# Performance work log

Hardware: AMD Instinct MI355X
Metric: run time of the kernel (lower is better)

The kernel has to match this reference:

```python
import jax, jax.numpy as jnp
import numpy as np

MODEL_DIM = 2048
Q_HEADS = 32
KV_HEADS = 8
HEAD_DIM = MODEL_DIM // Q_HEADS  # 64
ROPE_BASE = 10000.0


def apply_rope(x, pos):
    # x: [B, S, H, D], interleaved-pair RoPE (torchtune-style)
    half = x.shape[-1] // 2
    inv_freq = 1.0 / (ROPE_BASE ** (jnp.arange(half, dtype=jnp.float32) * 2.0 / x.shape[-1]))
    ang = pos.astype(jnp.float32)[:, None] * inv_freq[None, :]        # [S, half]
    cos = jnp.cos(ang)[None, :, None, :]                              # [1,S,1,half]
    sin = jnp.sin(ang)[None, :, None, :]
    x1 = x[..., 0::2]
    x2 = x[..., 1::2]
    o1 = x1 * cos - x2 * sin
    o2 = x2 * cos + x1 * sin
    return jnp.stack([o1, o2], axis=-1).reshape(x.shape)


def setup_inputs() -> dict:
    key = jax.random.key(0)
    ks = jax.random.split(key, 5)
    B, S, D = 2, 2048, MODEL_DIM
    sd = 1.0 / np.sqrt(D)
    x = jax.random.normal(ks[0], (B, S, D), dtype=jnp.float32)
    wq = jax.random.normal(ks[1], (Q_HEADS * HEAD_DIM, D), dtype=jnp.float32) * sd
    wk = jax.random.normal(ks[2], (KV_HEADS * HEAD_DIM, D), dtype=jnp.float32) * sd
    wv = jax.random.normal(ks[3], (KV_HEADS * HEAD_DIM, D), dtype=jnp.float32) * sd
    wo = jax.random.normal(ks[4], (D, D), dtype=jnp.float32) * sd
    attention_mask = jnp.ones((B, S), dtype=bool)
    return {"x": x, "attention_mask": attention_mask, "wq": wq, "wk": wk, "wv": wv, "wo": wo}


def reference(x, attention_mask, wq, wk, wv, wo):
    B, S, D = x.shape
    rep = Q_HEADS // KV_HEADS
    q = (x @ wq.T).reshape(B, S, Q_HEADS, HEAD_DIM)
    k = (x @ wk.T).reshape(B, S, KV_HEADS, HEAD_DIM)
    v = (x @ wv.T).reshape(B, S, KV_HEADS, HEAD_DIM)
    # GQA repeat_interleave along head axis
    k = jnp.repeat(k, rep, axis=2)
    v = jnp.repeat(v, rep, axis=2)
    pos = jnp.arange(S)
    q = apply_rope(q, pos)
    k = apply_rope(k, pos)
    # scores [B, H, Sq, Sk]
    score = jnp.einsum('bqhd,bkhd->bhqk', q, k) / np.sqrt(HEAD_DIM)
    neg_inf = jnp.finfo(score.dtype).min
    causal = jnp.tril(jnp.ones((S, S), dtype=bool))
    score = jnp.where(causal[None, None, :, :], score, neg_inf)
    score = jnp.where(attention_mask[:, None, None, :], score, neg_inf)
    attn = jax.nn.softmax(score, axis=-1)
    out = jnp.einsum('bhqk,bkhd->bqhd', attn, v).reshape(B, S, D)
    return out @ wo.T
```

## Files before the change

### kernel.cpp

```cpp
#include <hip/hip_runtime.h>
#include <hip/hip_bf16.h>

#define S_LEN 2048
#define BATCH 2
#define DMODEL 2048
#define HQ 32
#define HKV 8
#define HD 64
#define NQ 2560
#define KDIM 2048

typedef __attribute__((ext_vector_type(8))) short bf16x8;
typedef __attribute__((ext_vector_type(4))) float f32x4;

#if __has_builtin(__builtin_amdgcn_exp2f)
#define EXP2(x) __builtin_amdgcn_exp2f(x)
#else
#define EXP2(x) exp2f(x)
#endif

template<int N> struct ic { static constexpr int value = N; };

static __device__ inline ushort f2bf(float f) {
    union { float f; unsigned u; } v; v.f = f;
    unsigned r = v.u + 0x7fff + ((v.u >> 16) & 1);
    return (ushort)(r >> 16);
}
static __device__ inline float bf2f(ushort h) {
    union { unsigned u; float f; } v; v.u = ((unsigned)h) << 16; return v.f;
}
static __device__ inline unsigned pack2(float lo, float hi) {
    return (unsigned)f2bf(lo) | ((unsigned)f2bf(hi) << 16);
}
static __device__ __forceinline__ unsigned pkbf(float lo, float hi) {
    union { float f; unsigned u; } a, b; a.f = lo; b.f = hi;
    return __builtin_amdgcn_perm(b.u + 0x8000u, a.u + 0x8000u, 0x07060302u);
}
static __device__ __forceinline__ unsigned cvtpk(float lo, float hi) {
    unsigned r;
    asm("v_cvt_pk_bf16_f32 %0, %1, %2" : "=v"(r) : "v"(lo), "v"(hi));
    return r;
}

static __device__ __forceinline__ void gload16(const ushort* g, ushort* l) {
    __builtin_amdgcn_global_load_lds(
        (const __attribute__((address_space(1))) unsigned int*)(g),
        (__attribute__((address_space(3))) unsigned int*)(l), 16, 0, 0);
}

#define BARRIER() asm volatile("s_barrier" ::: "memory")
#define WAITVM(N) asm volatile("s_waitcnt vmcnt(" #N ")" ::: "memory")

__global__ __launch_bounds__(256) void convert_kernel(const float* __restrict__ x,
                                                      const float* __restrict__ wq,
                                                      const float* __restrict__ wk,
                                                      const float* __restrict__ wv,
                                                      const float* __restrict__ wo,
                                                      ushort* __restrict__ xb,
                                                      ushort* __restrict__ wqkvb,
                                                      ushort* __restrict__ wob)
{
    size_t e = ((size_t)blockIdx.x * 256 + threadIdx.x) * 8;
    const float* src; ushort* dst;
    if (e < 8388608ul)       { src = x  + e;              dst = xb + e; }
    else if (e < 12582912ul) { src = wq + (e - 8388608);  dst = wqkvb + (e - 8388608); }
    else if (e < 13631488ul) { src = wk + (e - 12582912); dst = wqkvb + 4194304 + (e - 12582912); }
    else if (e < 14680064ul) { src = wv + (e - 13631488); dst = wqkvb + 5242880 + (e - 13631488); }
    else                     { src = wo + (e - 14680064); dst = wob + (e - 14680064); }
    float4 a = *(const float4*)src;
    float4 b = *(const float4*)(src + 4);
    uint4 p; p.x = pack2(a.x, a.y); p.y = pack2(a.z, a.w);
             p.z = pack2(b.x, b.y); p.w = pack2(b.z, b.w);
    *(uint4*)dst = p;
}

template<int BNF, int EPI>
__global__ __launch_bounds__(512, 2) void gemm256(const ushort* __restrict__ A,
                                                  const ushort* __restrict__ Bw,
                                                  ushort* __restrict__ qkv,
                                                  ushort* __restrict__ vT,
                                                  float* __restrict__ Cf)
{
    constexpr int BN = BNF * 64;
    constexpr int KT = KDIM / 64;
    __shared__ ushort As[2][256 * 64];
    __shared__ ushort Bs[2][BN * 64];
    const int t    = threadIdx.x;
    const int w    = t >> 6, lane = t & 63;
    const int quad = lane >> 4, l15 = lane & 15;
    const int l8   = lane >> 3;
    const int scw  = ((lane & 7) ^ (l8 & 7)) * 8;
    const int wm   = (w >> 2) * 128;
    const int wn   = (w & 3) * (BNF * 16);

    const int bid = blockIdx.x;
    const int sb  = (bid & 7) * 32 + (bid >> 3);
    const int mb  = (sb >> 4) * 256;
    const int nb  = (sb & 15) * BN;

    f32x4 acc[8][BNF] = {};
    bf16x8 a[4][2], b[BNF][2];

    auto SAH = [&](int buf, int half, int kb) {
        #pragma unroll
        for (int L = 0; L < 2; L++) {
            int r0 = half * 128 + (w * 2 + L) * 8;
            gload16(A + (size_t)(mb + r0 + l8) * KDIM + kb + scw, &As[buf][r0 * 64]);
        }
    };
    auto SB = [&](int buf, int kb) {
        #pragma unroll
        for (int L = 0; L < BNF; L++) {
            int r0 = (w * BNF + L) * 8;
            gload16(Bw + (size_t)(nb + r0 + l8) * KDIM + kb + scw, &Bs[buf][r0 * 64]);
        }
    };
    auto LA = [&](int buf, int hm) {
        #pragma unroll
        for (int i = 0; i < 4; i++) {
            int r = wm + hm * 64 + i * 16 + l15;
            int rs = r * 64, sw = r & 7;
            #pragma unroll
            for (int kc = 0; kc < 2; kc++)
                a[i][kc] = *(const bf16x8*)&As[buf][rs + (((kc << 2) | quad) ^ sw) * 8];
        }
    };
    auto LB = [&](int buf) {
        #pragma unroll
        for (int j = 0; j < BNF; j++) {
            int r = wn + j * 16 + l15;
            int rs = r * 64, sw = r & 7;
            #pragma unroll
            for (int kc = 0; kc < 2; kc++)
                b[j][kc] = *(const bf16x8*)&Bs[buf][rs + (((kc << 2) | quad) ^ sw) * 8];
        }
    };
    auto MM = [&](auto HM) {
        constexpr int hm = decltype(HM)::value;
        __builtin_amdgcn_s_setprio(1);
        #pragma unroll
        for (int i = 0; i < 4; i++)
            #pragma unroll
            for (int j = 0; j < BNF; j++) {
                f32x4 d = acc[hm * 4 + i][j];
                d = __builtin_amdgcn_mfma_f32_16x16x32_bf16(a[i][0], b[j][0], d, 0, 0, 0);
                d = __builtin_amdgcn_mfma_f32_16x16x32_bf16(a[i][1], b[j][1], d, 0, 0, 0);
                acc[hm * 4 + i][j] = d;
            }
        __builtin_amdgcn_s_setprio(0);
    };

    SAH(0, 0, 0); SAH(0, 1, 0); SB(0, 0);
    SAH(1, 0, 64); SB(1, 64);
    if constexpr (BNF == 3) WAITVM(5); else WAITVM(4);
    BARRIER();

    #pragma unroll 1
    for (int tt = 0; tt < KT - 2; tt++) {
        const int buf = tt & 1, o = buf ^ 1;
        LA(buf, 0); LB(buf);
        SAH(o, 1, (tt + 1) * 64);
        BARRIER();
        MM(ic<0>{});
        if constexpr (BNF == 3) WAITVM(7); else WAITVM(6);
        BARRIER();
        LA(buf, 1);
        SAH(buf, 0, (tt + 2) * 64); SB(buf, (tt + 2) * 64);
        BARRIER();
        MM(ic<1>{});
        if constexpr (BNF == 3) WAITVM(7); else WAITVM(6);
        BARRIER();
    }
    LA(0, 0); LB(0);
    SAH(1, 1, (KT - 1) * 64);
    BARRIER();
    MM(ic<0>{});
    if constexpr (BNF == 3) WAITVM(7); else WAITVM(6);
    BARRIER();
    LA(0, 1);
    BARRIER();
    MM(ic<1>{});
    WAITVM(2);
    BARRIER();
    LA(1, 0); LB(1);
    BARRIER();
    MM(ic<0>{});
    WAITVM(0);
    BARRIER();
    LA(1, 1);
    BARRIER();
    MM(ic<1>{});

    #pragma unroll
    for (int i = 0; i < 8; i++) {
        int m0 = mb + wm + (i >> 2) * 64 + (i & 3) * 16 + quad * 4;
        #pragma unroll
        for (int j = 0; j < BNF; j++) {
            int n0 = nb + wn + j * 16;
            if (EPI == 0) {
                if (n0 >= 2560) {
                    int m0p = (m0 & ~63) | (((m0 >> 5) & 1) << 5)
                            | (((m0 >> 2) & 3) << 3) | (((m0 >> 4) & 1) << 2);
                    ushort4 pk;
                    pk.x = f2bf(acc[i][j][0]); pk.y = f2bf(acc[i][j][1]);
                    pk.z = f2bf(acc[i][j][2]); pk.w = f2bf(acc[i][j][3]);
                    *(ushort4*)&vT[(size_t)(n0 + l15 - 2560) * 4096 + m0p] = pk;
                } else {
                    #pragma unroll
                    for (int r = 0; r < 4; r++)
                        qkv[(size_t)(m0 + r) * NQ + n0 + l15] = f2bf(acc[i][j][r]);
                }
            } else {
                #pragma unroll
                for (int r = 0; r < 4; r++)
                    Cf[(size_t)(m0 + r) * DMODEL + n0 + l15] = acc[i][j][r];
            }
        }
    }
}

__global__ __launch_bounds__(256) void rope_kernel(ushort* __restrict__ qkv)
{
    const int PAIRS = BATCH * S_LEN * (HQ + HKV) * (HD / 2);
    int tid = blockIdx.x * 256 + threadIdx.x;
    if (tid >= PAIRS) return;
    int token = tid / ((HQ + HKV) * 32);
    int r     = tid - token * ((HQ + HKV) * 32);
    int hh    = r >> 5;
    int i     = r & 31;
    int base  = (hh < HQ) ? hh * 64 : DMODEL + (hh - HQ) * 64;
    size_t addr = (size_t)token * NQ + base + 2 * i;
    int s = token & (S_LEN - 1);
    float freq = exp2f(-0.41524101186092f * (float)i);
    float ang  = (float)s * freq;
    float sn, cs;
    sincosf(ang, &sn, &cs);
    float x1 = bf2f(qkv[addr]);
    float x2 = bf2f(qkv[addr + 1]);
    qkv[addr]     = f2bf(x1 * cs - x2 * sn);
    qkv[addr + 1] = f2bf(x2 * cs + x1 * sn);
}

__global__ __launch_bounds__(256) void attn_kernel(const ushort* __restrict__ qkv,
                                                   const ushort* __restrict__ vT,
                                                   ushort* __restrict__ attnb)
{
    __shared__ ushort Ks[2][64 * 64];
    __shared__ ushort VT[2][64 * 64];
    const int t    = threadIdx.x;
    const int w    = t >> 6, lane = t & 63;
    const int quad = lane >> 4, l15 = lane & 15;
    const int bid  = blockIdx.x;
    const int qx   = 15 - (bid >> 6);
    const int h    = bid & 31;
    const int b    = (bid >> 5) & 1;
    const int qb   = qx * 128;
    const int kvh  = h >> 2;
    const ushort* base = qkv + (size_t)b * S_LEN * NQ;
    const ushort* vTb  = vT + (size_t)kvh * HD * 4096 + b * S_LEN;

    const float SC = 0.18033688011112042f;
    bf16x8 aq[2][2];
    #pragma unroll
    for (int h2 = 0; h2 < 2; h2++) {
        const ushort* qp = base + (size_t)(qb + w * 32 + h2 * 16 + l15) * NQ + h * HD + quad * 8;
        #pragma unroll
        for (int hf = 0; hf < 2; hf++) {
            bf16x8 v = *(const bf16x8*)(qp + hf * 32);
            #pragma unroll
            for (int j = 0; j < 8; j++) v[j] = (short)f2bf(bf2f((ushort)v[j]) * SC);
            aq[h2][hf] = v;
        }
    }

    f32x4 o[2][4] = {};
    float lsum[2] = {};
    const int qw    = qb + w * 32;
    const int strow = lane >> 3;
    const int stlc  = (lane & 7) ^ strow;
    const int niter = (qb + 128) / 64;

    #pragma unroll
    for (int c = 0; c < 2; c++) {
        int key = w * 16 + c * 8 + strow;
        gload16(base + (size_t)key * NQ + DMODEL + kvh * HD + stlc * 8,
                &Ks[0][(w * 16 + c * 8) * 64]);
        gload16(vTb + (size_t)key * 4096 + stlc * 8,
                &VT[0][(w * 16 + c * 8) * 64]);
    }

    for (int i = 0; i < niter; i++) {
        const int kb  = i * 64;
        const int cur = i & 1;
        __syncthreads();
        if (i + 1 < niter) {
            int kb2 = kb + 64;
            #pragma unroll
            for (int c = 0; c < 2; c++) {
                int key = w * 16 + c * 8 + strow;
                gload16(base + (size_t)(kb2 + key) * NQ + DMODEL + kvh * HD + stlc * 8,
                        &Ks[1 - cur][(w * 16 + c * 8) * 64]);
                gload16(vTb + (size_t)key * 4096 + kb2 + stlc * 8,
                        &VT[1 - cur][(w * 16 + c * 8) * 64]);
            }
        }
        if (kb <= qw + 31) {
            const bool full = (kb + 63) <= qw;
            const ushort* ks = &Ks[cur][0];
            const ushort* vs = &VT[cur][0];
            f32x4 s[2][4];
            #pragma unroll
            for (int kt = 0; kt < 4; kt++) {
                int key = kt * 16 + l15;
                int sw  = l15 & 7;
                bf16x8 k0 = *(const bf16x8*)&ks[key * 64 + (quad ^ sw) * 8];
                bf16x8 k1 = *(const bf16x8*)&ks[key * 64 + (((quad + 4) & 7) ^ sw) * 8];
                #pragma unroll
                for (int h2 = 0; h2 < 2; h2++) {
                    f32x4 z = {};
                    z = __builtin_amdgcn_mfma_f32_16x16x32_bf16(k0, aq[h2][0], z, 0, 0, 0);
                    z = __builtin_amdgcn_mfma_f32_16x16x32_bf16(k1, aq[h2][1], z, 0, 0, 0);
                    s[h2][kt] = z;
                }
            }
            bf16x8 pf[2][2];
            #pragma unroll
            for (int h2 = 0; h2 < 2; h2++) {
                union { unsigned u[8]; bf16x8 v[2]; } pw;
                #pragma unroll
                for (int kt = 0; kt < 4; kt++) {
                    float p0 = EXP2(s[h2][kt][0]);
                    float p1 = EXP2(s[h2][kt][1]);
                    float p2 = EXP2(s[h2][kt][2]);
                    float p3 = EXP2(s[h2][kt][3]);
                    if (!full) {
                        int key0 = kb + kt * 16 + quad * 4;
                        int q    = qb + w * 32 + h2 * 16 + l15;
                        p0 = (key0 + 0 <= q) ? p0 : 0.f;
                        p1 = (key0 + 1 <= q) ? p1 : 0.f;
                        p2 = (key0 + 2 <= q) ? p2 : 0.f;
                        p3 = (key0 + 3 <= q) ? p3 : 0.f;
                    }
                    lsum[h2] += (p0 + p1) + (p2 + p3);
                    pw.u[kt * 2 + 0] = cvtpk(p0, p1);
                    pw.u[kt * 2 + 1] = cvtpk(p2, p3);
                }
                pf[h2][0] = pw.v[0];
                pf[h2][1] = pw.v[1];
            }
            #pragma unroll
            for (int tt = 0; tt < 4; tt++) {
                int dr = tt * 16 + l15;
                int sw = l15 & 7;
                bf16x8 vf0 = *(const bf16x8*)&vs[dr * 64 + (quad ^ sw) * 8];
                bf16x8 vf1 = *(const bf16x8*)&vs[dr * 64 + (((quad + 4) & 7) ^ sw) * 8];
                #pragma unroll
                for (int h2 = 0; h2 < 2; h2++) {
                    f32x4 oo = o[h2][tt];
                    oo = __builtin_amdgcn_mfma_f32_16x16x32_bf16(vf0, pf[h2][0], oo, 0, 0, 0);
                    oo = __builtin_amdgcn_mfma_f32_16x16x32_bf16(vf1, pf[h2][1], oo, 0, 0, 0);
                    o[h2][tt] = oo;
                }
            }
        }
    }
    #pragma unroll
    for (int h2 = 0; h2 < 2; h2++) {
        float l = lsum[h2];
        l += __shfl_xor(l, 16, 64);
        l += __shfl_xor(l, 32, 64);
        float inv = 1.0f / l;
        ushort* ob = attnb + (size_t)(b * S_LEN + qb + w * 32 + h2 * 16 + l15) * DMODEL
                   + h * HD + quad * 4;
        #pragma unroll
        for (int tt = 0; tt < 4; tt++) {
            uint2 st;
            st.x = pkbf(o[h2][tt][0] * inv, o[h2][tt][1] * inv);
            st.y = pkbf(o[h2][tt][2] * inv, o[h2][tt][3] * inv);
            *(uint2*)&ob[tt * 16] = st;
        }
    }
}

extern "C" void kernel_launch(void* const* d_in, const int* in_sizes, int n_in,
                              void* d_out, int out_size, void* d_ws, size_t ws_size,
                              hipStream_t stream)
{
    const float* x  = (const float*)d_in[0];
    const float* wq = (const float*)d_in[2];
    const float* wk = (const float*)d_in[3];
    const float* wv = (const float*)d_in[4];
    const float* wo = (const float*)d_in[5];
    float* out = (float*)d_out;

    char* ws = (char*)d_ws;
    ushort* qkv    = (ushort*)(ws);
    ushort* vT     = (ushort*)(ws + 20971520);
    ushort* xb     = (ushort*)(ws + 25165824);
    ushort* attn_b = xb;
    ushort* wqkvb  = (ushort*)(ws + 41943040);
    ushort* wob    = (ushort*)(ws + 54525952);

    convert_kernel<<<9216, 256, 0, stream>>>(x, wq, wk, wv, wo, xb, wqkvb, wob);

    gemm256<3, 0><<<256, 512, 0, stream>>>(xb, wqkvb, qkv, vT, nullptr);

    int pairs = BATCH * S_LEN * (HQ + HKV) * (HD / 2);
    rope_kernel<<<(pairs + 255) / 256, 256, 0, stream>>>(qkv);

    attn_kernel<<<1024, 256, 0, stream>>>(qkv, vT, attn_b);

    gemm256<2, 1><<<256, 512, 0, stream>>>(attn_b, wob, nullptr, nullptr, out);
}
```

Baseline: 268.4 us.

## Triple-buffer K tiles and use explicit vmcnt waits in attention loop

```diff
diff --git a/kernel.cpp b/kernel.cpp
--- a/kernel.cpp
+++ b/kernel.cpp
@@ -245,7 +245,7 @@
                                                    const ushort* __restrict__ vT,
                                                    ushort* __restrict__ attnb)
 {
-    __shared__ ushort Ks[2][64 * 64];
+    __shared__ ushort Ks[3][64 * 64];
     __shared__ ushort VT[2][64 * 64];
     const int t    = threadIdx.x;
     const int w    = t >> 6, lane = t & 63;
@@ -280,34 +280,36 @@
     const int stlc  = (lane & 7) ^ strow;
     const int niter = (qb + 128) / 64;
 
-    #pragma unroll
-    for (int c = 0; c < 2; c++) {
-        int key = w * 16 + c * 8 + strow;
-        gload16(base + (size_t)key * NQ + DMODEL + kvh * HD + stlc * 8,
-                &Ks[0][(w * 16 + c * 8) * 64]);
-        gload16(vTb + (size_t)key * 4096 + stlc * 8,
-                &VT[0][(w * 16 + c * 8) * 64]);
-    }
-
+    auto stageK = [&](int i, int buf) {
+        #pragma unroll
+        for (int c = 0; c < 2; c++) {
+            int key = w * 16 + c * 8 + strow;
+            gload16(base + (size_t)(i * 64 + key) * NQ + DMODEL + kvh * HD + stlc * 8,
+                    &Ks[buf][(w * 16 + c * 8) * 64]);
+        }
+    };
+    auto stageV = [&](int i, int buf) {
+        #pragma unroll
+        for (int c = 0; c < 2; c++) {
+            int key = w * 16 + c * 8 + strow;
+            gload16(vTb + (size_t)key * 4096 + i * 64 + stlc * 8,
+                    &VT[buf][(w * 16 + c * 8) * 64]);
+        }
+    };
+
+    stageK(0, 0); stageV(0, 0); stageK(1, 1);
+
+    int kcur = 0, vcur = 0;
     for (int i = 0; i < niter; i++) {
-        const int kb  = i * 64;
-        const int cur = i & 1;
-        __syncthreads();
-        if (i + 1 < niter) {
-            int kb2 = kb + 64;
-            #pragma unroll
-            for (int c = 0; c < 2; c++) {
-                int key = w * 16 + c * 8 + strow;
-                gload16(base + (size_t)(kb2 + key) * NQ + DMODEL + kvh * HD + stlc * 8,
-                        &Ks[1 - cur][(w * 16 + c * 8) * 64]);
-                gload16(vTb + (size_t)key * 4096 + kb2 + stlc * 8,
-                        &VT[1 - cur][(w * 16 + c * 8) * 64]);
-            }
-        }
+        const int kb = i * 64;
+        if (i + 1 < niter) { WAITVM(2); } else { WAITVM(0); }
+        BARRIER();
+        if (i + 1 < niter) stageV(i + 1, vcur ^ 1);
+        if (i + 2 < niter) stageK(i + 2, kcur >= 1 ? kcur - 1 : 2);
         if (kb <= qw + 31) {
             const bool full = (kb + 63) <= qw;
-            const ushort* ks = &Ks[cur][0];
-            const ushort* vs = &VT[cur][0];
+            const ushort* ks = &Ks[kcur][0];
+            const ushort* vs = &VT[vcur][0];
             f32x4 s[2][4];
             #pragma unroll
             for (int kt = 0; kt < 4; kt++) {
@@ -363,6 +365,8 @@
                 }
             }
         }
+        kcur = (kcur + 1 == 3) ? 0 : kcur + 1;
+        vcur ^= 1;
     }
     #pragma unroll
     for (int h2 = 0; h2 < 2; h2++) {
```

Result: no change. 272.8 us (+1.6%).

## Use 256-row query blocks with 8 waves in attention kernel

Applied to the files above, without the earlier changes.

```diff
diff --git a/kernel.cpp b/kernel.cpp
--- a/kernel.cpp
+++ b/kernel.cpp
@@ -241,9 +241,9 @@
     qkv[addr + 1] = f2bf(x2 * cs + x1 * sn);
 }
 
-__global__ __launch_bounds__(256) void attn_kernel(const ushort* __restrict__ qkv,
-                                                   const ushort* __restrict__ vT,
-                                                   ushort* __restrict__ attnb)
+__global__ __launch_bounds__(512, 4) void attn_kernel(const ushort* __restrict__ qkv,
+                                                      const ushort* __restrict__ vT,
+                                                      ushort* __restrict__ attnb)
 {
     __shared__ ushort Ks[2][64 * 64];
     __shared__ ushort VT[2][64 * 64];
@@ -251,10 +251,11 @@
     const int w    = t >> 6, lane = t & 63;
     const int quad = lane >> 4, l15 = lane & 15;
     const int bid  = blockIdx.x;
-    const int qx   = 15 - (bid >> 6);
+    const int g    = bid >> 6;
+    const int qs   = (g < 4) ? 7 - g : g - 4;
     const int h    = bid & 31;
     const int b    = (bid >> 5) & 1;
-    const int qb   = qx * 128;
+    const int qb   = qs * 256;
     const int kvh  = h >> 2;
     const ushort* base = qkv + (size_t)b * S_LEN * NQ;
     const ushort* vTb  = vT + (size_t)kvh * HD * 4096 + b * S_LEN;
@@ -278,32 +279,25 @@
     const int qw    = qb + w * 32;
     const int strow = lane >> 3;
     const int stlc  = (lane & 7) ^ strow;
-    const int niter = (qb + 128) / 64;
-
-    #pragma unroll
-    for (int c = 0; c < 2; c++) {
-        int key = w * 16 + c * 8 + strow;
-        gload16(base + (size_t)key * NQ + DMODEL + kvh * HD + stlc * 8,
-                &Ks[0][(w * 16 + c * 8) * 64]);
-        gload16(vTb + (size_t)key * 4096 + stlc * 8,
-                &VT[0][(w * 16 + c * 8) * 64]);
-    }
+    const int niter = (qb + 256) / 64;
+
+    auto stageK = [&](int i, int buf) {
+        gload16(base + (size_t)(i * 64 + w * 8 + strow) * NQ + DMODEL + kvh * HD + stlc * 8,
+                &Ks[buf][(w * 8) * 64]);
+    };
+    auto stageV = [&](int i, int buf) {
+        gload16(vTb + (size_t)(w * 8 + strow) * 4096 + i * 64 + stlc * 8,
+                &VT[buf][(w * 8) * 64]);
+    };
+
+    stageK(0, 0); stageV(0, 0);
 
     for (int i = 0; i < niter; i++) {
         const int kb  = i * 64;
         const int cur = i & 1;
-        __syncthreads();
-        if (i + 1 < niter) {
-            int kb2 = kb + 64;
-            #pragma unroll
-            for (int c = 0; c < 2; c++) {
-                int key = w * 16 + c * 8 + strow;
-                gload16(base + (size_t)(kb2 + key) * NQ + DMODEL + kvh * HD + stlc * 8,
-                        &Ks[1 - cur][(w * 16 + c * 8) * 64]);
-                gload16(vTb + (size_t)key * 4096 + kb2 + stlc * 8,
-                        &VT[1 - cur][(w * 16 + c * 8) * 64]);
-            }
-        }
+        WAITVM(0);
+        BARRIER();
+        if (i + 1 < niter) { stageV(i + 1, cur ^ 1); stageK(i + 1, cur ^ 1); }
         if (kb <= qw + 31) {
             const bool full = (kb + 63) <= qw;
             const ushort* ks = &Ks[cur][0];
@@ -408,7 +402,7 @@
     int pairs = BATCH * S_LEN * (HQ + HKV) * (HD / 2);
     rope_kernel<<<(pairs + 255) / 256, 256, 0, stream>>>(qkv);
 
-    attn_kernel<<<1024, 256, 0, stream>>>(qkv, vT, attn_b);
+    attn_kernel<<<512, 512, 0, stream>>>(qkv, vT, attn_b);
 
     gemm256<2, 1><<<256, 512, 0, stream>>>(attn_b, wob, nullptr, nullptr, out);
 }
```

New measurement: 271.2 us. Within noise of the previous version (+1.0%).
